# Optimization experiments

Hardware: AMD Instinct MI355X
Metric: run time of the kernel (lower is better)

Reference implementation:

```python
import jax, jax.numpy as jnp
import numpy as np

H = 16       # num_heads
HD = 64      # head_dim = embed_dim // num_heads
CLIP = 64    # clipping_threshold (Shaw et al. k)
B, L, D = 4, 1024, 1024


def setup_inputs() -> dict:
    key = jax.random.key(0)
    ks = jax.random.split(key, 13)
    f = lambda k_, s: jax.random.normal(k_, s, dtype=jnp.float32) * 0.02
    return {
        "q": f(ks[0], (B, L, D)),
        "k": f(ks[1], (B, L, D)),
        "v": f(ks[2], (B, L, D)),
        "Wq": f(ks[3], (D, D)), "bq": jnp.zeros((D,), jnp.float32),
        "Wk": f(ks[4], (D, D)), "bk": jnp.zeros((D,), jnp.float32),
        "Wv": f(ks[5], (D, D)), "bv": jnp.zeros((D,), jnp.float32),
        "Wo": f(ks[6], (D, D)), "bo": jnp.zeros((D,), jnp.float32),
        "Ek": f(ks[7], (2 * CLIP + 1, HD)),  # relative_position_k table
        "Ev": f(ks[8], (2 * CLIP + 1, HD)),  # relative_position_v table
    }


def reference(q, k, v, Wq, bq, Wk, bk, Wv, bv, Wo, bo, Ek, Ev):
    b, lq, d = q.shape
    lk = k.shape[1]
    # input projections (torch Linear: x @ W^T + b)
    qp = (q @ Wq.T + bq).reshape(b, lq, H, HD)
    kp = (k @ Wk.T + bk).reshape(b, lk, H, HD)
    vp = (v @ Wv.T + bv).reshape(b, lk, H, HD)
    # content-content scores
    attn1 = jnp.einsum("bqhd,bkhd->bhqk", qp, kp)
    # relative position embeddings R: (lq, lk, HD)
    idx = jnp.clip(jnp.arange(lk)[None, :] - jnp.arange(lq)[:, None], -CLIP, CLIP) + CLIP
    rel_k = Ek[idx]
    rel_v = Ev[idx]
    # content-position scores (Shaw et al. term added to QK^T)
    attn2 = jnp.einsum("bqhd,qkd->bhqk", qp, rel_k)
    scale = jnp.sqrt(jnp.asarray(HD, dtype=q.dtype))
    attn = jax.nn.softmax((attn1 + attn2) / scale, axis=-1)  # (b,H,lq,lk)
    # weighted values + relative value term
    out1 = jnp.einsum("bhqk,bkhd->bqhd", attn, vp)
    out2 = jnp.einsum("bhqk,qkd->bqhd", attn, rel_v)
    out = (out1 + out2).reshape(b, lq, d)
    return out @ Wo.T + bo
```

## Files before the change

kernel.cpp:

```cpp
#include <hip/hip_runtime.h>
#include <hip/hip_bf16.h>
#include <stdint.h>
#include <stddef.h>

#define B_ 4
#define L_ 1024
#define D_ 1024
#define H_ 16
#define HD_ 64
#define NROW 65536
#define QE_LD 132
#define EV_LD 192
#define T_STR 200

typedef __attribute__((ext_vector_type(8))) short bf16x8;
typedef __attribute__((ext_vector_type(4))) float f32x4;
typedef __attribute__((ext_vector_type(4))) unsigned short u16x4;

__device__ __forceinline__ float bf2f(unsigned short u) {
  union { unsigned int i; float f; } v; v.i = ((unsigned int)u) << 16; return v.f;
}
__device__ __forceinline__ unsigned short f2bf(float f) {
  union { float f; unsigned int i; } v; v.f = f;
  return (unsigned short)((v.i + 0x7fffu + ((v.i >> 16) & 1u)) >> 16);
}
__device__ __forceinline__ unsigned short f2bfrn(float f) {
  __hip_bfloat16 h = __float2bfloat16(f);
  return *reinterpret_cast<unsigned short*>(&h);
}
__device__ __forceinline__ void async16(const void* g, void* l) {
  __builtin_amdgcn_global_load_lds(
      (const __attribute__((address_space(1))) unsigned int*)g,
      (__attribute__((address_space(3))) unsigned int*)l, 16, 0, 0);
}

struct ConvArgs { const float* s[4]; unsigned short* d[4]; };

__global__ __launch_bounds__(256) void f32_to_bf16_multi(ConvArgs a, int n4) {
  const float* s = a.s[blockIdx.y];
  unsigned short* d = a.d[blockIdx.y];
  int i = blockIdx.x * 256 + threadIdx.x;
  int stride = gridDim.x * 256;
  for (; i < n4; i += stride) {
    float4 v = ((const float4*)s)[i];
    u16x4 o;
    o[0] = f2bf(v.x); o[1] = f2bf(v.y); o[2] = f2bf(v.z); o[3] = f2bf(v.w);
    ((u16x4*)d)[i] = o;
  }
}

__global__ __launch_bounds__(256) void build_ekev_k(const float* __restrict__ Ek,
                                                    const float* __restrict__ Ev,
                                                    unsigned short* __restrict__ Ekp,
                                                    unsigned short* __restrict__ EvTp) {
  int i = blockIdx.x * 256 + threadIdx.x;
  if (i < 256 * 64) {
    int r = i >> 6, dd = i & 63;
    Ekp[i] = (r < 129) ? f2bf(Ek[r * 64 + dd]) : (unsigned short)0;
  }
  if (i < 128 * EV_LD) {
    int dd = i / EV_LD, r = i - dd * EV_LD;
    EvTp[i] = (dd < 64 && r < 129) ? f2bf(Ev[r * 64 + dd]) : (unsigned short)0;
  }
}

struct Gemm3 {
  const unsigned short* A[3];
  const unsigned short* Bt[3];
  const float* bias[3];
  void* C[3];
};

template<int MI, bool OBF16, bool BIAS>
__global__ __launch_bounds__(256) void gemm_bt(Gemm3 ga, int lda, int ldb, int ldc,
                                               int Ncut, int ktiles) {
  constexpr int BM = MI * 32;
  __shared__ unsigned short Al[2][BM * 32];
  __shared__ unsigned short Bl[2][128 * 32];
  const unsigned short* A = ga.A[blockIdx.z];
  const unsigned short* Bt = ga.Bt[blockIdx.z];
  const float* bias = ga.bias[blockIdx.z];
  void* Cv = ga.C[blockIdx.z];
  const int tid = threadIdx.x;
  const int w = tid >> 6, l = tid & 63;
  const int l15 = l & 15, lg = l >> 4;
  const int row0 = blockIdx.x * BM, col0 = blockIdx.y * 128;
  const int wm = (w >> 1) * (MI * 16), wn = (w & 1) * 64;

  f32x4 acc[MI][4];
#pragma unroll
  for (int i = 0; i < MI; ++i)
#pragma unroll
    for (int j = 0; j < 4; ++j) acc[i][j] = {0.f, 0.f, 0.f, 0.f};

  auto stage = [&](int buf, int kt) {
#pragma unroll
    for (int i = 0; i < MI / 2; ++i) {
      int p = (i * 4 + w) * 1024 + l * 16;
      int m = p >> 6;
      int clog = (l & 3) ^ ((m >> 1) & 3);
      async16(A + (size_t)(row0 + m) * lda + kt * 32 + clog * 8,
              (char*)&Al[buf][0] + (i * 4 + w) * 1024);
    }
#pragma unroll
    for (int i = 0; i < 2; ++i) {
      int p = (i * 4 + w) * 1024 + l * 16;
      int m = p >> 6;
      int clog = (l & 3) ^ ((m >> 1) & 3);
      async16(Bt + (size_t)(col0 + m) * ldb + kt * 32 + clog * 8,
              (char*)&Bl[buf][0] + (i * 4 + w) * 1024);
    }
  };

  stage(0, 0);
  __syncthreads();
  for (int kt = 0; kt < ktiles; ++kt) {
    int cur = kt & 1;
    if (kt + 1 < ktiles) stage(cur ^ 1, kt + 1);
    bf16x8 af[MI], bfr[4];
#pragma unroll
    for (int mi = 0; mi < MI; ++mi) {
      int m = wm + mi * 16 + l15;
      af[mi] = *(const bf16x8*)&Al[cur][m * 32 + ((lg ^ ((m >> 1) & 3)) << 3)];
    }
#pragma unroll
    for (int ni = 0; ni < 4; ++ni) {
      int n = wn + ni * 16 + l15;
      bfr[ni] = *(const bf16x8*)&Bl[cur][n * 32 + ((lg ^ ((n >> 1) & 3)) << 3)];
    }
#pragma unroll
    for (int mi = 0; mi < MI; ++mi)
#pragma unroll
      for (int ni = 0; ni < 4; ++ni)
        acc[mi][ni] = __builtin_amdgcn_mfma_f32_16x16x32_bf16(af[mi], bfr[ni], acc[mi][ni], 0, 0, 0);
    __syncthreads();
  }

#pragma unroll
  for (int ni = 0; ni < 4; ++ni) {
    int col = col0 + wn + ni * 16 + l15;
    if (col < Ncut) {
      float bv = BIAS ? bias[col] : 0.f;
#pragma unroll
      for (int mi = 0; mi < MI; ++mi) {
        int rowb = row0 + wm + mi * 16 + lg * 4;
#pragma unroll
        for (int r = 0; r < 4; ++r) {
          float v = acc[mi][ni][r] + bv;
          size_t off = (size_t)(rowb + r) * ldc + col;
          if (OBF16) ((unsigned short*)Cv)[off] = f2bf(v);
          else       ((float*)Cv)[off] = v;
        }
      }
    }
  }
}

__global__ __launch_bounds__(256) void transpose_v_k(const unsigned short* __restrict__ vp,
                                                     unsigned short* __restrict__ vpT) {
  const int lt = blockIdx.x, bh = blockIdx.y;
  const int b = bh >> 4, h = bh & 15;
  __shared__ unsigned short tile[64][72];
  const int t = threadIdx.x;
#pragma unroll
  for (int j = 0; j < 2; ++j) {
    int lrow = (t >> 3) + 32 * j;
    int d0 = (t & 7) * 8;
    bf16x8 v = *(const bf16x8*)(vp + ((size_t)((b * L_ + lt * 64 + lrow) * H_ + h)) * HD_ + d0);
#pragma unroll
    for (int e = 0; e < 8; ++e) tile[lrow][d0 + e] = (unsigned short)v[e];
  }
  __syncthreads();
#pragma unroll
  for (int j = 0; j < 2; ++j) {
    int d = (t >> 3) + 32 * j;
    int l0 = (t & 7) * 8;
    bf16x8 o;
#pragma unroll
    for (int e = 0; e < 8; ++e) o[e] = (short)tile[l0 + e][d];
    *(bf16x8*)(vpT + ((size_t)((b * H_ + h) * HD_ + d)) * L_ + lt * 64 + l0) = o;
  }
}

__global__ __launch_bounds__(256, 3) void flash_fwd_k(
    const unsigned short* __restrict__ qp, const unsigned short* __restrict__ kp,
    const unsigned short* __restrict__ vpT, const unsigned short* __restrict__ qE,
    const unsigned short* __restrict__ EvTp, unsigned short* __restrict__ tmp) {
  __shared__ __align__(16) char smem[40960];
  unsigned short (*Kl)[4096] = (unsigned short (*)[4096])smem;
  unsigned short (*Vl)[4096] = (unsigned short (*)[4096])(smem + 16384);
  const int tid = threadIdx.x, w = tid >> 6, l = tid & 63;
  unsigned short* Plw = (unsigned short*)(smem + 32768) + w * 1024;
  const int l15 = l & 15, lg = l >> 4;
  const int bid = blockIdx.x;
  const int bh = bid & 63, qt = bid >> 6;
  const int b = bh >> 4, h = bh & 15;
  const int qw = qt * 64 + w * 16;
  const int q_lane = qw + l15;
  const int rowbase = (b * L_ + qw) * H_ + h;
  const int rowi_lane = rowbase + l15 * H_;
  constexpr float C1 = 0.125f * 1.44269504f;

  bf16x8 qf[2];
  {
    const unsigned short* qrp = qp + (size_t)rowi_lane * HD_;
#pragma unroll
    for (int ks = 0; ks < 2; ++ks) qf[ks] = *(const bf16x8*)(qrp + ks * 32 + lg * 8);
  }
  const unsigned short* qerow = qE + (size_t)rowi_lane * QE_LD;
  const float qe0L = bf2f(qerow[0]) * C1;
  const float qe128L = bf2f(qerow[128]) * C1;

  f32x4 O[4];
#pragma unroll
  for (int nd = 0; nd < 4; ++nd) O[nd] = {0.f, 0.f, 0.f, 0.f};
  float mrow = -1e30f, lrow = 0.f, t0row = 0.f;

  u16x4 pks0[4], pks1[4], pks2[4];
  float mu0 = -1e30f, mu1 = -1e30f, mu2 = -1e30f;
  {
    u16x4 z4 = {0, 0, 0, 0};
#pragma unroll
    for (int ni = 0; ni < 4; ++ni) { pks0[ni] = z4; pks1[ni] = z4; pks2[ni] = z4; }
  }

  auto stage = [&](int buf, int kt) {
#pragma unroll
    for (int i = 0; i < 2; ++i) {
      int p = (i * 4 + w) * 1024 + l * 16;
      int row = p >> 7;
      int clog = (l & 7) ^ (row & 7);
      async16(kp + ((size_t)((b * L_ + kt * 64 + row) * H_ + h)) * HD_ + clog * 8,
              (char*)&Kl[buf][0] + (i * 4 + w) * 1024);
      async16(vpT + ((size_t)((b * H_ + h) * HD_ + row)) * L_ + kt * 64 + clog * 8,
              (char*)&Vl[buf][0] + (i * 4 + w) * 1024);
    }
  };

  stage(0, 0);
  __syncthreads();

  for (int kt = 0; kt < 16; ++kt) {
    int cur = kt & 1;
    if (kt + 1 < 16) stage(cur ^ 1, kt + 1);

    f32x4 S[4];
#pragma unroll
    for (int ni = 0; ni < 4; ++ni) S[ni] = {0.f, 0.f, 0.f, 0.f};
#pragma unroll
    for (int ks = 0; ks < 2; ++ks) {
      bf16x8 kf[4];
#pragma unroll
      for (int ni = 0; ni < 4; ++ni) {
        int kk = ni * 16 + l15;
        kf[ni] = *(const bf16x8*)&Kl[cur][kk * 64 + (((ks * 4 + lg) ^ (kk & 7)) << 3)];
      }
#pragma unroll
      for (int ni = 0; ni < 4; ++ni)
        S[ni] = __builtin_amdgcn_mfma_f32_16x16x32_bf16(kf[ni], qf[ks], S[ni], 0, 0, 0);
    }

    const int cls = (kt <= qt - 2) ? 0 : ((kt >= qt + 2) ? 2 : 1);
    const int based = kt * 64 - q_lane;

    if (cls == 1) {
#pragma unroll
      for (int ni = 0; ni < 4; ++ni)
#pragma unroll
        for (int r = 0; r < 4; ++r) {
          int delta = based + ni * 16 + lg * 4 + r;
          int idx = min(max(delta, -64), 64) + 64;
          S[ni][r] = S[ni][r] * C1 + bf2f(qerow[idx]) * C1;
        }
    } else {
      float qeL = (cls == 0) ? qe0L : qe128L;
#pragma unroll
      for (int ni = 0; ni < 4; ++ni)
#pragma unroll
        for (int r = 0; r < 4; ++r) S[ni][r] = S[ni][r] * C1 + qeL;
    }

    float x0 = fmaxf(fmaxf(S[0][0], S[0][1]), fmaxf(S[0][2], S[0][3]));
    float x1 = fmaxf(fmaxf(S[1][0], S[1][1]), fmaxf(S[1][2], S[1][3]));
    float x2 = fmaxf(fmaxf(S[2][0], S[2][1]), fmaxf(S[2][2], S[2][3]));
    float x3 = fmaxf(fmaxf(S[3][0], S[3][1]), fmaxf(S[3][2], S[3][3]));
    float pmax = fmaxf(fmaxf(x0, x1), fmaxf(x2, x3));
    pmax = fmaxf(pmax, __shfl_xor(pmax, 16));
    pmax = fmaxf(pmax, __shfl_xor(pmax, 32));

    float a = 1.f;
    if (!__all(pmax <= mrow + 11.54f)) {
      float mnew = fmaxf(mrow, pmax);
      a = __builtin_amdgcn_exp2f(mrow - mnew);
      mrow = mnew;
      float aq0 = __shfl(a, lg * 4 + 0);
      float aq1 = __shfl(a, lg * 4 + 1);
      float aq2 = __shfl(a, lg * 4 + 2);
      float aq3 = __shfl(a, lg * 4 + 3);
#pragma unroll
      for (int nd = 0; nd < 4; ++nd) {
        O[nd][0] *= aq0; O[nd][1] *= aq1; O[nd][2] *= aq2; O[nd][3] *= aq3;
      }
    }

#pragma unroll
    for (int ni = 0; ni < 4; ++ni)
#pragma unroll
      for (int r = 0; r < 4; ++r)
        S[ni][r] = __builtin_amdgcn_exp2f(S[ni][r] - mrow);

    float s0 = (S[0][0] + S[0][1]) + (S[0][2] + S[0][3]);
    float s1 = (S[1][0] + S[1][1]) + (S[1][2] + S[1][3]);
    float s2 = (S[2][0] + S[2][1]) + (S[2][2] + S[2][3]);
    float s3 = (S[3][0] + S[3][1]) + (S[3][2] + S[3][3]);
    float ps = (s0 + s1) + (s2 + s3);
    ps += __shfl_xor(ps, 16);
    ps += __shfl_xor(ps, 32);
    lrow = lrow * a + ps;

    if (cls == 0) {
      t0row = t0row * a + ps;
    } else if (cls == 2) {
      t0row = t0row * a;
    } else if (kt == qt - 1) {
      float p0 = 0.f;
#pragma unroll
      for (int ni = 0; ni < 4; ++ni)
#pragma unroll
        for (int r = 0; r < 4; ++r)
          if (based + ni * 16 + lg * 4 + r <= -64) p0 += S[ni][r];
      p0 += __shfl_xor(p0, 16);
      p0 += __shfl_xor(p0, 32);
      t0row = t0row * a + p0;
    } else {
      t0row = t0row * a;
    }

    u16x4 pcur[4];
#pragma unroll
    for (int ni = 0; ni < 4; ++ni) {
      u16x4 pk;
#pragma unroll
      for (int r = 0; r < 4; ++r) pk[r] = f2bfrn(S[ni][r]);
      pcur[ni] = pk;
      int slot = (ni * 2 + (lg >> 1)) ^ (l15 & 7);
      int addr = l15 * 64 + (slot << 3) + (lg & 1) * 4;
      *(u16x4*)&Plw[addr] = pk;
    }
    if (cls == 1) {
      if (kt == qt - 1) {
#pragma unroll
        for (int ni = 0; ni < 4; ++ni) pks0[ni] = pcur[ni];
        mu0 = mrow;
      } else if (kt == qt) {
#pragma unroll
        for (int ni = 0; ni < 4; ++ni) pks1[ni] = pcur[ni];
        mu1 = mrow;
      } else {
#pragma unroll
        for (int ni = 0; ni < 4; ++ni) pks2[ni] = pcur[ni];
        mu2 = mrow;
      }
    }

#pragma unroll
    for (int ks = 0; ks < 2; ++ks) {
      bf16x8 pf = *(const bf16x8*)&Plw[l15 * 64 + (((ks * 4 + lg) ^ (l15 & 7)) << 3)];
      bf16x8 vf[4];
#pragma unroll
      for (int nd = 0; nd < 4; ++nd) {
        int d = nd * 16 + l15;
        vf[nd] = *(const bf16x8*)&Vl[cur][d * 64 + (((ks * 4 + lg) ^ (d & 7)) << 3)];
      }
#pragma unroll
      for (int nd = 0; nd < 4; ++nd)
        O[nd] = __builtin_amdgcn_mfma_f32_16x16x32_bf16(pf, vf[nd], O[nd], 0, 0, 0);
    }
    __syncthreads();
  }

  unsigned short* Tl16 = (unsigned short*)smem + w * (16 * T_STR);
  {
    u16x4 z4 = {0, 0, 0, 0};
    u16x4* tl4 = (u16x4*)Tl16;
    for (int i = l; i < 16 * T_STR / 4; i += 64) tl4[i] = z4;
  }
  float bandsum = 0.f;
  auto addband = [&](const u16x4* pk, float muv, int btc) {
    float scale = __builtin_amdgcn_exp2f(muv - mrow);
    int jbase = (qt + btc - 1) * 64 + lg * 4 - q_lane + 64;
#pragma unroll
    for (int ni = 0; ni < 4; ++ni)
#pragma unroll
      for (int r = 0; r < 4; ++r) {
        int j = jbase + ni * 16 + r;
        if (j >= 1 && j <= 127) {
          float pf = bf2f((unsigned short)pk[ni][r]) * scale;
          Tl16[l15 * T_STR + j] = f2bfrn(pf);
          bandsum += pf;
        }
      }
  };
  addband(pks0, mu0, 0);
  addband(pks1, mu1, 1);
  addband(pks2, mu2, 2);
  bandsum += __shfl_xor(bandsum, 16);
  bandsum += __shfl_xor(bandsum, 32);
  if (lg == 0) {
    Tl16[l15 * T_STR] = f2bfrn(t0row);
    Tl16[l15 * T_STR + 128] = f2bfrn(fmaxf(0.f, lrow - t0row - bandsum));
  }
#pragma unroll
  for (int ks6 = 0; ks6 < 6; ++ks6) {
    bf16x8 af = *(const bf16x8*)(Tl16 + l15 * T_STR + ks6 * 32 + lg * 8);
    bf16x8 bfr[4];
#pragma unroll
    for (int nd = 0; nd < 4; ++nd)
      bfr[nd] = *(const bf16x8*)(EvTp + (size_t)(nd * 16 + l15) * EV_LD + ks6 * 32 + lg * 8);
#pragma unroll
    for (int nd = 0; nd < 4; ++nd)
      O[nd] = __builtin_amdgcn_mfma_f32_16x16x32_bf16(af, bfr[nd], O[nd], 0, 0, 0);
  }

  float invl = 1.f / lrow;
  float iq[4];
#pragma unroll
  for (int r = 0; r < 4; ++r) iq[r] = __shfl(invl, lg * 4 + r);
#pragma unroll
  for (int r = 0; r < 4; ++r) {
    size_t rowi = (size_t)(rowbase + (lg * 4 + r) * H_);
#pragma unroll
    for (int nd = 0; nd < 4; ++nd)
      tmp[rowi * HD_ + nd * 16 + l15] = f2bfrn(O[nd][r] * iq[r]);
  }
}

extern "C" void kernel_launch(void* const* d_in, const int* in_sizes, int n_in,
                              void* d_out, int out_size, void* d_ws, size_t ws_size,
                              hipStream_t stream) {
  (void)in_sizes; (void)n_in; (void)out_size; (void)ws_size;
  const float* q  = (const float*)d_in[0];
  const float* k  = (const float*)d_in[1];
  const float* v  = (const float*)d_in[2];
  const float* Wq = (const float*)d_in[3];
  const float* bq = (const float*)d_in[4];
  const float* Wk = (const float*)d_in[5];
  const float* bk = (const float*)d_in[6];
  const float* Wv = (const float*)d_in[7];
  const float* bv = (const float*)d_in[8];
  const float* Wo = (const float*)d_in[9];
  const float* bo = (const float*)d_in[10];
  const float* Ek = (const float*)d_in[11];
  const float* Ev = (const float*)d_in[12];

  char* ws = (char*)d_ws;
  constexpr size_t SZ_QKV = (size_t)B_ * L_ * D_ * 2;
  constexpr size_t SZ_W   = (size_t)D_ * D_ * 2;
  constexpr size_t OFF_QB = 0;
  constexpr size_t OFF_KB = OFF_QB + SZ_QKV;
  constexpr size_t OFF_VB = OFF_KB + SZ_QKV;
  constexpr size_t OFF_WQ = OFF_VB + SZ_QKV;
  constexpr size_t OFF_WK = OFF_WQ + SZ_W;
  constexpr size_t OFF_WV = OFF_WK + SZ_W;
  constexpr size_t OFF_QE = OFF_WV + SZ_W;
  constexpr size_t OFF_WO = OFF_QE + (size_t)NROW * QE_LD * 2;
  constexpr size_t OFF_EKP = OFF_WO + SZ_W;
  constexpr size_t OFF_EVT = OFF_EKP + 256 * 64 * 2;
  constexpr size_t OFF_QP = OFF_EVT + 128 * EV_LD * 2;
  constexpr size_t OFF_KP = OFF_QP + SZ_QKV;
  constexpr size_t OFF_VP = OFF_KP + SZ_QKV;
  constexpr size_t OFF_VPT = OFF_VP + SZ_QKV;
  constexpr size_t OFF_TMP = OFF_VPT + SZ_QKV;

  auto U16 = [&](size_t off) { return (unsigned short*)(ws + off); };

  {
    ConvArgs a{};
    a.s[0] = q; a.s[1] = k; a.s[2] = v;
    a.d[0] = U16(OFF_QB); a.d[1] = U16(OFF_KB); a.d[2] = U16(OFF_VB);
    f32_to_bf16_multi<<<dim3(2048, 3), 256, 0, stream>>>(a, (B_ * L_ * D_) / 4);
    ConvArgs bargs{};
    bargs.s[0] = Wq; bargs.s[1] = Wk; bargs.s[2] = Wv; bargs.s[3] = Wo;
    bargs.d[0] = U16(OFF_WQ); bargs.d[1] = U16(OFF_WK); bargs.d[2] = U16(OFF_WV); bargs.d[3] = U16(OFF_WO);
    f32_to_bf16_multi<<<dim3(1024, 4), 256, 0, stream>>>(bargs, (D_ * D_) / 4);
  }
  build_ekev_k<<<96, 256, 0, stream>>>(Ek, Ev, U16(OFF_EKP), U16(OFF_EVT));

  {
    Gemm3 g{};
    g.A[0] = U16(OFF_QB); g.Bt[0] = U16(OFF_WQ); g.bias[0] = bq; g.C[0] = U16(OFF_QP);
    g.A[1] = U16(OFF_KB); g.Bt[1] = U16(OFF_WK); g.bias[1] = bk; g.C[1] = U16(OFF_KP);
    g.A[2] = U16(OFF_VB); g.Bt[2] = U16(OFF_WV); g.bias[2] = bv; g.C[2] = U16(OFF_VP);
    gemm_bt<4, true, true><<<dim3(32, 8, 3), 256, 0, stream>>>(g, 1024, 1024, 1024, 1024, 32);
  }

  transpose_v_k<<<dim3(16, 64), 256, 0, stream>>>(U16(OFF_VP), U16(OFF_VPT));

  {
    Gemm3 g{};
    g.A[0] = U16(OFF_QP); g.Bt[0] = U16(OFF_EKP); g.bias[0] = nullptr; g.C[0] = U16(OFF_QE);
    gemm_bt<2, true, false><<<dim3(1024, 2, 1), 256, 0, stream>>>(g, 64, 64, QE_LD, 129, 2);
  }

  flash_fwd_k<<<1024, 256, 0, stream>>>(
      U16(OFF_QP), U16(OFF_KP), U16(OFF_VPT), U16(OFF_QE), U16(OFF_EVT), U16(OFF_TMP));

  {
    Gemm3 g{};
    g.A[0] = U16(OFF_TMP); g.Bt[0] = U16(OFF_WO); g.bias[0] = bo; g.C[0] = d_out;
    gemm_bt<2, false, true><<<dim3(64, 8, 1), 256, 0, stream>>>(g, 1024, 1024, 1024, 1024, 32);
  }
}
```

Baseline: 147.1 us.

## Raise occupancy in flash and GEMM kernels and merge conversion launches

```diff
diff --git a/kernel.cpp b/kernel.cpp
--- a/kernel.cpp
+++ b/kernel.cpp
@@ -34,11 +34,13 @@
       (__attribute__((address_space(3))) unsigned int*)l, 16, 0, 0);
 }
 
-struct ConvArgs { const float* s[4]; unsigned short* d[4]; };
-
-__global__ __launch_bounds__(256) void f32_to_bf16_multi(ConvArgs a, int n4) {
-  const float* s = a.s[blockIdx.y];
-  unsigned short* d = a.d[blockIdx.y];
+struct ConvArgs7 { const float* s[7]; unsigned short* d[7]; int n4[7]; };
+
+__global__ __launch_bounds__(256) void f32_to_bf16_multi(ConvArgs7 a) {
+  const int y = blockIdx.y;
+  const float* s = a.s[y];
+  unsigned short* d = a.d[y];
+  const int n4 = a.n4[y];
   int i = blockIdx.x * 256 + threadIdx.x;
   int stride = gridDim.x * 256;
   for (; i < n4; i += stride) {
@@ -72,9 +74,10 @@
 };
 
 template<int MI, bool OBF16, bool BIAS>
-__global__ __launch_bounds__(256) void gemm_bt(Gemm3 ga, int lda, int ldb, int ldc,
-                                               int Ncut, int ktiles) {
+__global__ __launch_bounds__(256, 4) void gemm_bt(Gemm3 ga, int lda, int ldb, int ldc,
+                                                  int Ncut, int ktiles) {
   constexpr int BM = MI * 32;
+  constexpr int AI = MI / 2;
   __shared__ unsigned short Al[2][BM * 32];
   __shared__ unsigned short Bl[2][128 * 32];
   const unsigned short* A = ga.A[blockIdx.z];
@@ -95,7 +98,7 @@
 
   auto stage = [&](int buf, int kt) {
 #pragma unroll
-    for (int i = 0; i < MI / 2; ++i) {
+    for (int i = 0; i < AI; ++i) {
       int p = (i * 4 + w) * 1024 + l * 16;
       int m = p >> 6;
       int clog = (l & 3) ^ ((m >> 1) & 3);
@@ -182,15 +185,14 @@
   }
 }
 
-__global__ __launch_bounds__(256, 3) void flash_fwd_k(
+__global__ __launch_bounds__(256, 4) void flash_fwd_k(
     const unsigned short* __restrict__ qp, const unsigned short* __restrict__ kp,
     const unsigned short* __restrict__ vpT, const unsigned short* __restrict__ qE,
     const unsigned short* __restrict__ EvTp, unsigned short* __restrict__ tmp) {
-  __shared__ __align__(16) char smem[40960];
+  __shared__ __align__(16) char smem[32768];
   unsigned short (*Kl)[4096] = (unsigned short (*)[4096])smem;
   unsigned short (*Vl)[4096] = (unsigned short (*)[4096])(smem + 16384);
   const int tid = threadIdx.x, w = tid >> 6, l = tid & 63;
-  unsigned short* Plw = (unsigned short*)(smem + 32768) + w * 1024;
   const int l15 = l & 15, lg = l >> 4;
   const int bid = blockIdx.x;
   const int bh = bid & 63, qt = bid >> 6;
@@ -335,6 +337,11 @@
     } else {
       t0row = t0row * a;
     }
+
+    asm volatile("" ::: "memory");
+    __builtin_amdgcn_s_barrier();
+    asm volatile("" ::: "memory");
+    unsigned short* Plw = (unsigned short*)(smem + cur * 8192) + w * 1024;
 
     u16x4 pcur[4];
 #pragma unroll
@@ -462,11 +469,11 @@
   constexpr size_t OFF_WQ = OFF_VB + SZ_QKV;
   constexpr size_t OFF_WK = OFF_WQ + SZ_W;
   constexpr size_t OFF_WV = OFF_WK + SZ_W;
-  constexpr size_t OFF_QE = OFF_WV + SZ_W;
-  constexpr size_t OFF_WO = OFF_QE + (size_t)NROW * QE_LD * 2;
+  constexpr size_t OFF_WO = OFF_WV + SZ_W;
   constexpr size_t OFF_EKP = OFF_WO + SZ_W;
   constexpr size_t OFF_EVT = OFF_EKP + 256 * 64 * 2;
-  constexpr size_t OFF_QP = OFF_EVT + 128 * EV_LD * 2;
+  constexpr size_t OFF_QE = OFF_EVT + 128 * EV_LD * 2;
+  constexpr size_t OFF_QP = OFF_QE + (size_t)NROW * QE_LD * 2;
   constexpr size_t OFF_KP = OFF_QP + SZ_QKV;
   constexpr size_t OFF_VP = OFF_KP + SZ_QKV;
   constexpr size_t OFF_VPT = OFF_VP + SZ_QKV;
@@ -475,14 +482,15 @@
   auto U16 = [&](size_t off) { return (unsigned short*)(ws + off); };
 
   {
-    ConvArgs a{};
-    a.s[0] = q; a.s[1] = k; a.s[2] = v;
-    a.d[0] = U16(OFF_QB); a.d[1] = U16(OFF_KB); a.d[2] = U16(OFF_VB);
-    f32_to_bf16_multi<<<dim3(2048, 3), 256, 0, stream>>>(a, (B_ * L_ * D_) / 4);
-    ConvArgs bargs{};
-    bargs.s[0] = Wq; bargs.s[1] = Wk; bargs.s[2] = Wv; bargs.s[3] = Wo;
-    bargs.d[0] = U16(OFF_WQ); bargs.d[1] = U16(OFF_WK); bargs.d[2] = U16(OFF_WV); bargs.d[3] = U16(OFF_WO);
-    f32_to_bf16_multi<<<dim3(1024, 4), 256, 0, stream>>>(bargs, (D_ * D_) / 4);
+    ConvArgs7 c{};
+    c.s[0] = q;  c.d[0] = U16(OFF_QB); c.n4[0] = (B_ * L_ * D_) / 4;
+    c.s[1] = k;  c.d[1] = U16(OFF_KB); c.n4[1] = (B_ * L_ * D_) / 4;
+    c.s[2] = v;  c.d[2] = U16(OFF_VB); c.n4[2] = (B_ * L_ * D_) / 4;
+    c.s[3] = Wq; c.d[3] = U16(OFF_WQ); c.n4[3] = (D_ * D_) / 4;
+    c.s[4] = Wk; c.d[4] = U16(OFF_WK); c.n4[4] = (D_ * D_) / 4;
+    c.s[5] = Wv; c.d[5] = U16(OFF_WV); c.n4[5] = (D_ * D_) / 4;
+    c.s[6] = Wo; c.d[6] = U16(OFF_WO); c.n4[6] = (D_ * D_) / 4;
+    f32_to_bf16_multi<<<dim3(1024, 7), 256, 0, stream>>>(c);
   }
   build_ekev_k<<<96, 256, 0, stream>>>(Ek, Ev, U16(OFF_EKP), U16(OFF_EVT));
 
@@ -491,7 +499,7 @@
     g.A[0] = U16(OFF_QB); g.Bt[0] = U16(OFF_WQ); g.bias[0] = bq; g.C[0] = U16(OFF_QP);
     g.A[1] = U16(OFF_KB); g.Bt[1] = U16(OFF_WK); g.bias[1] = bk; g.C[1] = U16(OFF_KP);
     g.A[2] = U16(OFF_VB); g.Bt[2] = U16(OFF_WV); g.bias[2] = bv; g.C[2] = U16(OFF_VP);
-    gemm_bt<4, true, true><<<dim3(32, 8, 3), 256, 0, stream>>>(g, 1024, 1024, 1024, 1024, 32);
+    gemm_bt<2, true, true><<<dim3(64, 8, 3), 256, 0, stream>>>(g, 1024, 1024, 1024, 1024, 32);
   }
 
   transpose_v_k<<<dim3(16, 64), 256, 0, stream>>>(U16(OFF_VP), U16(OFF_VPT));
```

After: 154.1 us. 4.7% more time.
